# Optimization experiments

Hardware: AMD Instinct MI355X
Metric: run time of the kernel (lower is better)

## Reference

```python
import jax, jax.numpy as jnp
import numpy as np

D, H, W = 8, 64, 64  # image_shape
EPS = 1e-6
LOG_2PI = float(np.log(2.0 * np.pi))


def _pixel_positions():
    z = jnp.arange(D, dtype=jnp.float32) - (D - 1) / 2.0
    y = jnp.arange(H, dtype=jnp.float32) - (H - 1) / 2.0
    x = jnp.arange(W, dtype=jnp.float32) - (W - 1) / 2.0
    zg, yg, xg = jnp.meshgrid(z, y, x, indexing='ij')  # [D,H,W]
    return jnp.stack([xg, yg, zg], axis=-1).reshape(-1, 3)  # [N,3], order (x,y,z)


def setup_inputs() -> dict:
    key = jax.random.key(0)
    ks = jax.random.split(key, 5)
    return {
        'representation': jax.random.normal(ks[0], (1024, 256), dtype=jnp.float32),
        'mean_W': jax.random.normal(ks[1], (3, 256), dtype=jnp.float32) * 0.05,
        'mean_b': jax.random.normal(ks[2], (3,), dtype=jnp.float32) * 0.05,
        'scale_W': jax.random.normal(ks[3], (6, 256), dtype=jnp.float32) * 0.05,
        'scale_b': jax.random.normal(ks[4], (6,), dtype=jnp.float32) * 0.05,
    }


def reference(representation, mean_W, mean_b, scale_W, scale_b):
    # tiny projections
    means = representation @ mean_W.T + mean_b          # [B,3]
    raw = representation @ scale_W.T + scale_b          # [B,6]
    s = jax.nn.softplus(raw) + EPS                      # softplus in forward
    # FillScaleTriL: vec -> lower-tri (row-major: (0,0),(1,0),(1,1),(2,0),(2,1),(2,2)),
    # then softplus applied again to the diagonal only.
    L00 = jax.nn.softplus(s[:, 0])
    L10 = s[:, 1]
    L11 = jax.nn.softplus(s[:, 2])
    L20 = s[:, 3]
    L21 = s[:, 4]
    L22 = jax.nn.softplus(s[:, 5])

    pix = _pixel_positions()                            # [N,3]
    diff = pix[None, :, :] - means[:, None, :]          # [B,N,3]
    # hardcoded 3x3 forward-substitution: y = L^{-1} diff
    y0 = diff[..., 0] / L00[:, None]
    y1 = (diff[..., 1] - L10[:, None] * y0) / L11[:, None]
    y2 = (diff[..., 2] - L20[:, None] * y0 - L21[:, None] * y1) / L22[:, None]
    maha = y0 * y0 + y1 * y1 + y2 * y2                  # [B,N]
    log_det = jnp.log(L00) + jnp.log(L11) + jnp.log(L22)  # [B]
    log_probs = -0.5 * maha - log_det[:, None] - 1.5 * LOG_2PI  # [B,N]

    log_probs_stable = log_probs - jnp.max(log_probs, axis=1, keepdims=True)
    profile = jnp.exp(log_probs_stable)
    profile = profile / (jnp.sum(profile, axis=1, keepdims=True) + 1e-10)
    return profile
```

## Files before the change

### kernel.cpp

```cpp
#include <hip/hip_runtime.h>
#include <math.h>

#define NG    1024
#define KD    256
#define NPIX  32768
#define BLOCK 512
#define PT    64

#define C_15_LOG2PI 2.7568155996140185f

__device__ __forceinline__ float softplus_f(float x) {
    return fmaxf(x, 0.0f) + log1pf(expf(-fabsf(x)));
}

__global__ __launch_bounds__(BLOCK)
void mvn_profile_kernel(const float* __restrict__ rep,
                        const float* __restrict__ mean_W,
                        const float* __restrict__ mean_b,
                        const float* __restrict__ scale_W,
                        const float* __restrict__ scale_b,
                        float* __restrict__ out)
{
    const int g = blockIdx.x;
    const int t = threadIdx.x;

    __shared__ float s_part[9][4];
    __shared__ float s_par[10];
    __shared__ float s_red[8];

    if (t < KD) {
        float r = rep[g * KD + t];
        float acc[9];
        #pragma unroll
        for (int k = 0; k < 3; ++k) acc[k]     = r * mean_W[k * KD + t];
        #pragma unroll
        for (int k = 0; k < 6; ++k) acc[3 + k] = r * scale_W[k * KD + t];
        #pragma unroll
        for (int k = 0; k < 9; ++k) {
            float v = acc[k];
            #pragma unroll
            for (int off = 32; off >= 1; off >>= 1)
                v += __shfl_xor(v, off, 64);
            if ((t & 63) == 0) s_part[k][t >> 6] = v;
        }
    }
    __syncthreads();
    if (t == 0) {
        float dsum[9];
        #pragma unroll
        for (int k = 0; k < 9; ++k)
            dsum[k] = (s_part[k][0] + s_part[k][1]) + (s_part[k][2] + s_part[k][3]);
        float mx = dsum[0] + mean_b[0];
        float my = dsum[1] + mean_b[1];
        float mz = dsum[2] + mean_b[2];
        float s0 = softplus_f(dsum[3] + scale_b[0]) + 1e-6f;
        float s1 = softplus_f(dsum[4] + scale_b[1]) + 1e-6f;
        float s2 = softplus_f(dsum[5] + scale_b[2]) + 1e-6f;
        float s3 = softplus_f(dsum[6] + scale_b[3]) + 1e-6f;
        float s4 = softplus_f(dsum[7] + scale_b[4]) + 1e-6f;
        float s5 = softplus_f(dsum[8] + scale_b[5]) + 1e-6f;
        float L00 = softplus_f(s0);
        float L11 = softplus_f(s2);
        float L22 = softplus_f(s5);
        s_par[0] = mx; s_par[1] = my; s_par[2] = mz;
        s_par[3] = 1.0f / L00;
        s_par[4] = s1;
        s_par[5] = 1.0f / L11;
        s_par[6] = s3;
        s_par[7] = s4;
        s_par[8] = 1.0f / L22;
        s_par[9] = logf(L00) + logf(L11) + logf(L22) + C_15_LOG2PI;
    }
    __syncthreads();
    const float mx  = s_par[0], my  = s_par[1], mz  = s_par[2];
    const float r00 = s_par[3], L10 = s_par[4], r11 = s_par[5];
    const float L20 = s_par[6], L21 = s_par[7], r22 = s_par[8];
    const float c   = s_par[9];

    const float px    = (float)(t & 63) - 31.5f;
    const float y0    = (px - mx) * r00;
    const float negc2 = -(c + 0.5f * y0 * y0);
    const float dyoff = -31.5f - my - L10 * y0;
    const float dzoff = -3.5f  - mz - L20 * y0;

    float lp[PT];
    float lmax = -3.4e38f;
    const int jbase = t >> 6;
    #pragma unroll
    for (int i = 0; i < PT; ++i) {
        int   j  = jbase + 8 * i;
        float fy = (float)(j & 63);
        float fz = (float)(j >> 6);
        float y1 = (fy + dyoff) * r11;
        float w  = fz + dzoff - L21 * y1;
        float y2 = w * r22;
        float q  = y1 * y1 + y2 * y2;
        float v  = fmaf(-0.5f, q, negc2);
        lp[i] = v;
        lmax = fmaxf(lmax, v);
    }

    #pragma unroll
    for (int off = 32; off >= 1; off >>= 1)
        lmax = fmaxf(lmax, __shfl_xor(lmax, off, 64));
    if ((t & 63) == 0) s_red[t >> 6] = lmax;
    __syncthreads();
    float m = s_red[0];
    #pragma unroll
    for (int k = 1; k < 8; ++k) m = fmaxf(m, s_red[k]);

    float lsum = 0.0f;
    #pragma unroll
    for (int i = 0; i < PT; ++i) {
        float e = __expf(lp[i] - m);
        lp[i] = e;
        lsum += e;
    }
    #pragma unroll
    for (int off = 32; off >= 1; off >>= 1)
        lsum += __shfl_xor(lsum, off, 64);
    __syncthreads();
    if ((t & 63) == 0) s_red[t >> 6] = lsum;
    __syncthreads();
    float S = 0.0f;
    #pragma unroll
    for (int k = 0; k < 8; ++k) S += s_red[k];
    const float scale = 1.0f / (S + 1e-10f);

    float* op = out + (size_t)g * NPIX + t;
    #pragma unroll
    for (int i = 0; i < PT; ++i)
        op[i * BLOCK] = lp[i] * scale;
}

extern "C" void kernel_launch(void* const* d_in, const int* in_sizes, int n_in,
                              void* d_out, int out_size, void* d_ws, size_t ws_size,
                              hipStream_t stream) {
    const float* rep     = (const float*)d_in[0];
    const float* mean_W  = (const float*)d_in[1];
    const float* mean_b  = (const float*)d_in[2];
    const float* scale_W = (const float*)d_in[3];
    const float* scale_b = (const float*)d_in[4];
    float* out = (float*)d_out;

    hipLaunchKernelGGL(mvn_profile_kernel, dim3(NG), dim3(BLOCK), 0, stream,
                       rep, mean_W, mean_b, scale_W, scale_b, out);
}
```

Before: 151.2 us.

## Drop max pass, recompute exponentials in log2 domain with float4 stores

Removes the 64-element register array and the block-wide max reduction. Each thread now owns four x-consecutive pixels and precomputes per-row terms. The softmax is done as a sum pass of exp2 values followed by a recompute pass that folds log2 of the sum into the exponent and writes float4 vectors. This lowers register pressure (launch bounds now request 8 waves), halves the barriers and vectorizes the stores, at the cost of evaluating every exponential twice. Skipping the max subtraction relies on the log-probabilities not underflowing or overflowing, which holds only because the constant normalization is folded in.

```diff
diff --git a/kernel.cpp b/kernel.cpp
--- a/kernel.cpp
+++ b/kernel.cpp
@@ -5,15 +5,24 @@
 #define KD    256
 #define NPIX  32768
 #define BLOCK 512
-#define PT    64
 
-#define C_15_LOG2PI 2.7568155996140185f
+#define LN2PI_15  2.7568155996140185f
+#define LOG2E     1.4426950408889634f
+#define SQH_L2E   0.8493218f
 
 __device__ __forceinline__ float softplus_f(float x) {
     return fmaxf(x, 0.0f) + log1pf(expf(-fabsf(x)));
 }
 
-__global__ __launch_bounds__(BLOCK)
+__device__ __forceinline__ float exp2_fast(float x) {
+#if __has_builtin(__builtin_amdgcn_exp2f)
+    return __builtin_amdgcn_exp2f(x);
+#else
+    float r; asm("v_exp_f32 %0, %1" : "=v"(r) : "v"(x)); return r;
+#endif
+}
+
+__global__ __launch_bounds__(BLOCK, 8)
 void mvn_profile_kernel(const float* __restrict__ rep,
                         const float* __restrict__ mean_W,
                         const float* __restrict__ mean_b,
@@ -30,14 +39,14 @@
 
     if (t < KD) {
         float r = rep[g * KD + t];
-        float acc[9];
+        float acc9[9];
         #pragma unroll
-        for (int k = 0; k < 3; ++k) acc[k]     = r * mean_W[k * KD + t];
+        for (int k = 0; k < 3; ++k) acc9[k]     = r * mean_W[k * KD + t];
         #pragma unroll
-        for (int k = 0; k < 6; ++k) acc[3 + k] = r * scale_W[k * KD + t];
+        for (int k = 0; k < 6; ++k) acc9[3 + k] = r * scale_W[k * KD + t];
         #pragma unroll
         for (int k = 0; k < 9; ++k) {
-            float v = acc[k];
+            float v = acc9[k];
             #pragma unroll
             for (int off = 32; off >= 1; off >>= 1)
                 v += __shfl_xor(v, off, 64);
@@ -68,69 +77,84 @@
         s_par[5] = 1.0f / L11;
         s_par[6] = s3;
         s_par[7] = s4;
-        s_par[8] = 1.0f / L22;
-        s_par[9] = logf(L00) + logf(L11) + logf(L22) + C_15_LOG2PI;
+        s_par[8] = SQH_L2E / L22;
+        s_par[9] = -LOG2E * (logf(L00) + logf(L11) + logf(L22) + LN2PI_15);
     }
     __syncthreads();
-    const float mx  = s_par[0], my  = s_par[1], mz  = s_par[2];
-    const float r00 = s_par[3], L10 = s_par[4], r11 = s_par[5];
-    const float L20 = s_par[6], L21 = s_par[7], r22 = s_par[8];
-    const float c   = s_par[9];
+    const float mx   = s_par[0], my  = s_par[1], mz  = s_par[2];
+    const float r00  = s_par[3], L10 = s_par[4], r11 = s_par[5];
+    const float L20  = s_par[6], L21 = s_par[7], r22s = s_par[8];
+    const float c0   = s_par[9];
+    const float mzc  = -3.5f - mz;
 
-    const float px    = (float)(t & 63) - 31.5f;
-    const float y0    = (px - mx) * r00;
-    const float negc2 = -(c + 0.5f * y0 * y0);
-    const float dyoff = -31.5f - my - L10 * y0;
-    const float dzoff = -3.5f  - mz - L20 * y0;
-
-    float lp[PT];
-    float lmax = -3.4e38f;
-    const int jbase = t >> 6;
+    const float xb = (float)(4 * (t & 15)) - 31.5f - mx;
+    const float f0 = (float)(t >> 4);
+    float urs[8], base[8];
     #pragma unroll
-    for (int i = 0; i < PT; ++i) {
-        int   j  = jbase + 8 * i;
-        float fy = (float)(j & 63);
-        float fz = (float)(j >> 6);
-        float y1 = (fy + dyoff) * r11;
-        float w  = fz + dzoff - L21 * y1;
-        float y2 = w * r22;
-        float q  = y1 * y1 + y2 * y2;
-        float v  = fmaf(-0.5f, q, negc2);
-        lp[i] = v;
-        lmax = fmaxf(lmax, v);
+    for (int k = 0; k < 4; ++k) {
+        float y0  = (xb + (float)k) * r00;
+        float y0s = y0 * SQH_L2E;
+        float b0  = fmaf(-y0s, y0s, c0);
+        float dzk = fmaf(-L20, y0, mzc);
+        float dyk = fmaf(-L10, y0, -31.5f - my);
+        #pragma unroll
+        for (int f = 0; f < 2; ++f) {
+            float py  = f0 + (float)(32 * f);
+            float y1  = (py + dyk) * r11;
+            float y1s = y1 * SQH_L2E;
+            base[k*2+f] = fmaf(-y1s, y1s, b0);
+            urs [k*2+f] = fmaf(-L21, y1, dzk) * r22s;
+        }
     }
 
+    float acc0 = 0.f, acc1 = 0.f, acc2 = 0.f, acc3 = 0.f;
     #pragma unroll
-    for (int off = 32; off >= 1; off >>= 1)
-        lmax = fmaxf(lmax, __shfl_xor(lmax, off, 64));
-    if ((t & 63) == 0) s_red[t >> 6] = lmax;
-    __syncthreads();
-    float m = s_red[0];
-    #pragma unroll
-    for (int k = 1; k < 8; ++k) m = fmaxf(m, s_red[k]);
-
-    float lsum = 0.0f;
-    #pragma unroll
-    for (int i = 0; i < PT; ++i) {
-        float e = __expf(lp[i] - m);
-        lp[i] = e;
-        lsum += e;
+    for (int i = 0; i < 16; ++i) {
+        const int   fs = i & 1;
+        const float fz = (float)(i >> 1);
+        {
+            float y2s = fmaf(fz, r22s, urs[0*2+fs]);
+            acc0 += exp2_fast(fmaf(-y2s, y2s, base[0*2+fs]));
+        }
+        {
+            float y2s = fmaf(fz, r22s, urs[1*2+fs]);
+            acc1 += exp2_fast(fmaf(-y2s, y2s, base[1*2+fs]));
+        }
+        {
+            float y2s = fmaf(fz, r22s, urs[2*2+fs]);
+            acc2 += exp2_fast(fmaf(-y2s, y2s, base[2*2+fs]));
+        }
+        {
+            float y2s = fmaf(fz, r22s, urs[3*2+fs]);
+            acc3 += exp2_fast(fmaf(-y2s, y2s, base[3*2+fs]));
+        }
     }
+    float lsum = (acc0 + acc1) + (acc2 + acc3);
     #pragma unroll
     for (int off = 32; off >= 1; off >>= 1)
         lsum += __shfl_xor(lsum, off, 64);
-    __syncthreads();
     if ((t & 63) == 0) s_red[t >> 6] = lsum;
     __syncthreads();
     float S = 0.0f;
     #pragma unroll
     for (int k = 0; k < 8; ++k) S += s_red[k];
-    const float scale = 1.0f / (S + 1e-10f);
 
-    float* op = out + (size_t)g * NPIX + t;
+    const float lS = log2f(S + 1e-10f);
     #pragma unroll
-    for (int i = 0; i < PT; ++i)
-        op[i * BLOCK] = lp[i] * scale;
+    for (int k = 0; k < 8; ++k) base[k] -= lS;
+
+    float4* op4 = (float4*)(out + (size_t)g * NPIX) + t;
+    #pragma unroll
+    for (int i = 0; i < 16; ++i) {
+        const int   fs = i & 1;
+        const float fz = (float)(i >> 1);
+        float4 o;
+        { float y2s = fmaf(fz, r22s, urs[0*2+fs]); o.x = exp2_fast(fmaf(-y2s, y2s, base[0*2+fs])); }
+        { float y2s = fmaf(fz, r22s, urs[1*2+fs]); o.y = exp2_fast(fmaf(-y2s, y2s, base[1*2+fs])); }
+        { float y2s = fmaf(fz, r22s, urs[2*2+fs]); o.z = exp2_fast(fmaf(-y2s, y2s, base[2*2+fs])); }
+        { float y2s = fmaf(fz, r22s, urs[3*2+fs]); o.w = exp2_fast(fmaf(-y2s, y2s, base[3*2+fs])); }
+        op4[i * 512] = o;
+    }
 }
 
 extern "C" void kernel_launch(void* const* d_in, const int* in_sizes, int n_in,
```

After: 169.7 us. +12.2%, slower.
